# Performance work log

Measured on AMD Instinct MI355X. Metric: run time of the kernel, lower is better.

Reference implementation:

```python
import jax, jax.numpy as jnp
import numpy as np

B, D, E, K = 32768, 512, 64, 4
NCTX = 16
H = (NCTX // 2 - 1) * 768  # 5376: per-expert context block, (n_ctx/2 - 1) rows of ctx_dim=768
NOISE_EPS = 1e-2
LOSS_COEF = 1e-2


def setup_inputs() -> dict:
    key = jax.random.key(0)
    ks = jax.random.split(key, 5)
    x = jax.random.normal(ks[0], (B, D), jnp.float32)
    w_gate = jax.random.normal(ks[1], (D, E), jnp.float32) * 0.02
    w_noise = jax.random.normal(ks[2], (D, E), jnp.float32) * 0.02
    noise = jax.random.normal(ks[3], (B, E), jnp.float32)
    ctx_c = jax.random.normal(ks[4], (E, H), jnp.float32) * 0.02
    return {"x": x, "w_gate": w_gate, "w_noise": w_noise, "noise": noise, "ctx_c": ctx_c}


def _cv_squared(v, eps=1e-10):
    # coefficient-of-variation squared: var / mean^2
    return jnp.var(v) / (jnp.mean(v) ** 2 + eps)


def _normal_cdf(z):
    return 0.5 * (1.0 + jax.lax.erf(z * (1.0 / np.sqrt(2.0))))


def reference(x, w_gate, w_noise, noise, ctx_c):
    # ---- noisy top-k gating (Shazeer sparsely-gated MoE) ----
    clean_logits = x @ w_gate                                    # [B, E]
    noise_stddev = jax.nn.softplus(x @ w_noise) + NOISE_EPS      # [B, E]
    noisy_logits = clean_logits + noise * noise_stddev           # [B, E]

    top_logits, top_idx = jax.lax.top_k(noisy_logits, K + 1)     # [B, K+1]
    top_k_logits = top_logits[:, :K]
    top_k_idx = top_idx[:, :K]
    top_k_gates = jax.nn.softmax(top_k_logits, axis=-1)          # [B, K]

    rows = jnp.arange(B)[:, None]
    gates = jnp.zeros((B, E), x.dtype).at[rows, top_k_idx].set(top_k_gates)  # sparse -> dense scatter

    # ---- load-balancing aux loss ----
    importance = gates.sum(axis=0)                               # [E]
    thr_in = top_logits[:, K][:, None]                           # (K+1)-th largest noisy logit
    thr_out = top_logits[:, K - 1][:, None]                      # K-th largest noisy logit
    is_in = noisy_logits > thr_in
    prob_in = _normal_cdf((clean_logits - thr_in) / noise_stddev)
    prob_out = _normal_cdf((clean_logits - thr_out) / noise_stddev)
    load = jnp.where(is_in, prob_in, prob_out).sum(axis=0)       # [E]
    aux_loss = (_cv_squared(importance) + _cv_squared(load)) * LOSS_COEF

    # ---- weighted combine of per-expert context vectors (as in LPromptLearner) ----
    out = jnp.einsum('be,eh->bh', gates, ctx_c)                  # [B, H]
    return out, aux_loss
```

## Files before the change

kernel.cpp:

```cpp
#include <hip/hip_runtime.h>
#include <math.h>

#define B_ 32768
#define D_ 512
#define E_ 64
#define H_ 5376
#define H4_ (H_ / 4)
#define HC_ 128
#define NCH_ (H_ / HC_)

typedef float f32x4 __attribute__((ext_vector_type(4)));
typedef _Float16 f16x8 __attribute__((ext_vector_type(8)));
typedef unsigned int u32x4 __attribute__((ext_vector_type(4)));

__device__ __forceinline__ unsigned short f16bits(_Float16 h) {
    union { _Float16 h; unsigned short u; } c; c.h = h; return c.u;
}

__global__ __launch_bounds__(256) void prep_kernel(
    const float* __restrict__ wgate, const float* __restrict__ wnoise,
    _Float16* __restrict__ wt0, _Float16* __restrict__ wt1)
{
    int e = blockIdx.x;
    int n  = e >> 4, le = e & 15;
    const float* src = (e < E_) ? (wgate + e) : (wnoise + (e - E_));
    for (int k = threadIdx.x; k < D_; k += 256) {
        float v = src[(size_t)k * E_] * 1024.0f;
        _Float16 h0 = (_Float16)v;
        _Float16 h1 = (_Float16)(v - (float)h0);
        int ks = k >> 5, g = (k & 31) >> 3, j = k & 7;
        size_t idx = ((size_t)(ks * 8 + n) * 64 + g * 16 + le) * 8 + j;
        wt0[idx] = h0;
        wt1[idx] = h1;
    }
}

#define TOP5_STEP(TV, TI)                                              \
    {                                                                  \
        double bm = v0; int bj = 0;                                    \
        if (v1 > bm) { bm = v1; bj = 1; }                              \
        if (v2 > bm) { bm = v2; bj = 2; }                              \
        if (v3 > bm) { bm = v3; bj = 3; }                              \
        int be = bj * 16 + le;                                         \
        _Pragma("unroll")                                              \
        for (int off = 1; off < 16; off <<= 1) {                       \
            double om = __shfl_xor(bm, off, 64);                       \
            int    oe = __shfl_xor(be, off, 64);                       \
            if (om > bm || (om == bm && oe < be)) { bm = om; be = oe; }\
        }                                                              \
        TV = bm; TI = be;                                              \
        bool wn = ((be & 15) == le); int sl = be >> 4;                 \
        v0 = (wn && sl == 0) ? -1.0e300 : v0;                          \
        v1 = (wn && sl == 1) ? -1.0e300 : v1;                          \
        v2 = (wn && sl == 2) ? -1.0e300 : v2;                          \
        v3 = (wn && sl == 3) ? -1.0e300 : v3;                          \
    }

#define ISSUE_LOADS(Q)                                                         \
    _Pragma("unroll")                                                          \
    for (int i = 0; i < 4; ++i) {                                              \
        int id  = t + 256 * i;                                                 \
        const float* src = x + (size_t)(b0 + (id >> 4)) * D_ + (Q) * 128 +     \
                           (id & 15) * 8;                                      \
        ra[2 * i]     = *(const float4*)src;                                   \
        ra[2 * i + 1] = *(const float4*)(src + 4);                             \
    }

#define CONVERT_WRITE(BUF)                                                     \
    _Pragma("unroll")                                                          \
    for (int i = 0; i < 4; ++i) {                                              \
        int id  = t + 256 * i;                                                 \
        int row = id >> 4;                                                     \
        int c   = id & 15;                                                     \
        float vv[8] = {ra[2*i].x, ra[2*i].y, ra[2*i].z, ra[2*i].w,             \
                       ra[2*i+1].x, ra[2*i+1].y, ra[2*i+1].z, ra[2*i+1].w};    \
        unsigned int hw[4], lw[4];                                             \
        _Pragma("unroll")                                                      \
        for (int p = 0; p < 4; ++p) {                                          \
            float va = vv[2*p] * 16.0f, vb = vv[2*p+1] * 16.0f;                \
            _Float16 a0 = (_Float16)va, b0f = (_Float16)vb;                    \
            _Float16 a1 = (_Float16)((va - (float)a0) * 4096.0f);              \
            _Float16 b1 = (_Float16)((vb - (float)b0f) * 4096.0f);             \
            hw[p] = (unsigned)f16bits(a0) | ((unsigned)f16bits(b0f) << 16);    \
            lw[p] = (unsigned)f16bits(a1) | ((unsigned)f16bits(b1) << 16);     \
        }                                                                      \
        int addr = (row * 256 + c * 16) ^ ((row & 7) << 4);                    \
        *(u32x4*)((char*)x0s[BUF] + addr) = (u32x4){hw[0], hw[1], hw[2], hw[3]};\
        *(u32x4*)((char*)x1s[BUF] + addr) = (u32x4){lw[0], lw[1], lw[2], lw[3]};\
    }

__global__ __launch_bounds__(256) void gate_kernel(
    const float* __restrict__ x,
    const _Float16* __restrict__ wt0,
    const _Float16* __restrict__ wt1,
    const float* __restrict__ noise,
    unsigned int* __restrict__ o_idx,
    float4* __restrict__ o_g,
    float* __restrict__ g_imp,
    float* __restrict__ g_load)
{
    __shared__ __align__(16) _Float16 x0s[2][64 * 128];
    __shared__ __align__(16) _Float16 x1s[2][64 * 128];
    __shared__ float s_imp[E_];
    __shared__ float s_load[E_];

    const int t  = threadIdx.x;
    const int w  = t >> 6;
    const int l  = t & 63;
    const int le = l & 15;
    const int g  = l >> 4;
    const int b0 = blockIdx.x * 64;
    const int arow = w * 16 + le;

    if (t < E_) { s_imp[t] = 0.0f; s_load[t] = 0.0f; }

    f32x4 accAC[8], accB[8];
#pragma unroll
    for (int n = 0; n < 8; ++n) {
        accAC[n] = (f32x4){0.f, 0.f, 0.f, 0.f};
        accB[n]  = (f32x4){0.f, 0.f, 0.f, 0.f};
    }

    float4 ra[8];
    ISSUE_LOADS(0)
    CONVERT_WRITE(0)

#pragma unroll
    for (int q = 0; q < 4; ++q) {
        if (q < 3) ISSUE_LOADS(q + 1)
        __syncthreads();
#pragma unroll
        for (int s = 0; s < 4; ++s) {
            int aoff = (arow * 256 + s * 64 + g * 16) ^ ((arow & 7) << 4);
            f16x8 a0 = *(const f16x8*)((const char*)x0s[q & 1] + aoff);
            f16x8 a1 = *(const f16x8*)((const char*)x1s[q & 1] + aoff);
            int ks = q * 4 + s;
#pragma unroll
            for (int n = 0; n < 8; ++n) {
                size_t boff = ((size_t)(ks * 8 + n) * 64 + l) * 8;
                f16x8 b0 = *(const f16x8*)(wt0 + boff);
                f16x8 b1 = *(const f16x8*)(wt1 + boff);
                accAC[n] = __builtin_amdgcn_mfma_f32_16x16x32_f16(a0, b0, accAC[n], 0, 0, 0);
                accAC[n] = __builtin_amdgcn_mfma_f32_16x16x32_f16(a0, b1, accAC[n], 0, 0, 0);
                accB[n]  = __builtin_amdgcn_mfma_f32_16x16x32_f16(a1, b0, accB[n],  0, 0, 0);
            }
        }
        if (q < 3) CONVERT_WRITE((q + 1) & 1)
    }

    const double UNSCALE = 1.0 / 16384.0;
    const double RESC    = 1.0 / 4096.0;
    float loadacc[4] = {0.f, 0.f, 0.f, 0.f};
#pragma unroll
    for (int r = 0; r < 4; ++r) {
        int li = w * 16 + g * 4 + r;
        int b  = b0 + li;
        double cl[4], ny[4];
        float  sdf[4];
#pragma unroll
        for (int n = 0; n < 4; ++n) {
            cl[n] = ((double)accAC[n][r] + (double)accB[n][r] * RESC) * UNSCALE;
            float z = (float)(((double)accAC[n+4][r] + (double)accB[n+4][r] * RESC) * UNSCALE);
            float sp = (z > 20.0f) ? z : log1pf(expf(z));
            sdf[n] = sp + 0.01f;
            float nz = noise[(size_t)b * E_ + le + 16 * n];
            ny[n] = cl[n] + (double)(nz * sdf[n]);
        }
        double v0 = ny[0], v1 = ny[1], v2 = ny[2], v3 = ny[3];
        double tv0, tv1, tv2, tv3, tv4;
        int    ti0, ti1, ti2, ti3, ti4;
        TOP5_STEP(tv0, ti0)
        TOP5_STEP(tv1, ti1)
        TOP5_STEP(tv2, ti2)
        TOP5_STEP(tv3, ti3)
        TOP5_STEP(tv4, ti4)
        float e1 = expf((float)(tv1 - tv0)),
              e2 = expf((float)(tv2 - tv0)),
              e3 = expf((float)(tv3 - tv0));
        float inv = 1.0f / (1.0f + e1 + e2 + e3);
        float g0 = inv, g1 = e1 * inv, g2 = e2 * inv, g3 = e3 * inv;
        if (le == 0) {
            o_idx[b] = (unsigned)ti0 | ((unsigned)ti1 << 8) |
                       ((unsigned)ti2 << 16) | ((unsigned)ti3 << 24);
            float4 gv; gv.x = g0; gv.y = g1; gv.z = g2; gv.w = g3;
            o_g[b] = gv;
            atomicAdd(&s_imp[ti0], g0);
            atomicAdd(&s_imp[ti1], g1);
            atomicAdd(&s_imp[ti2], g2);
            atomicAdd(&s_imp[ti3], g3);
        }
        double thr_out = tv3;
        double thr_in  = tv4;
#pragma unroll
        for (int n = 0; n < 4; ++n) {
            double thr = (ny[n] > thr_in) ? thr_in : thr_out;
            float  zz  = (float)(cl[n] - thr) / sdf[n];
            loadacc[n] += 0.5f * (1.0f + erff(zz * 0.70710678118654752f));
        }
    }
#pragma unroll
    for (int n = 0; n < 4; ++n) atomicAdd(&s_load[16 * n + le], loadacc[n]);
    __syncthreads();
    if (t < E_) {
        atomicAdd(&g_imp[t],  s_imp[t]);
        atomicAdd(&g_load[t], s_load[t]);
    }
}

__global__ __launch_bounds__(256) void dispatch_kernel(
    const float* __restrict__ ctx,
    const unsigned int* __restrict__ o_idx,
    const float4* __restrict__ o_g,
    float* __restrict__ out)
{
    __shared__ f32x4 cs[E_ * (HC_ / 4)];

    const int t  = threadIdx.x;
    const int h0 = blockIdx.x * HC_;
    const int tb = blockIdx.y * 64;

#pragma unroll
    for (int i = 0; i < 8; ++i) {
        int idx = t + 256 * i;
        int e = idx >> 5, c = idx & 31;
        cs[idx] = *(const f32x4*)&ctx[(size_t)e * H_ + h0 + c * 4];
    }
    __syncthreads();

    const int tok = t >> 5;
    const int c   = t & 31;
#pragma unroll
    for (int s = 0; s < 8; ++s) {
        int b = tb + s * 8 + tok;
        unsigned pk = o_idx[b];
        float4 g = o_g[b];
        f32x4 r = g.x * cs[((pk      ) & 255u) * 32 + c]
                + g.y * cs[((pk >>  8) & 255u) * 32 + c]
                + g.z * cs[((pk >> 16) & 255u) * 32 + c]
                + g.w * cs[( pk >> 24         ) * 32 + c];
        __builtin_nontemporal_store(r, (f32x4*)&out[(size_t)b * H_ + h0 + c * 4]);
    }
}

__global__ void loss_kernel(const float* __restrict__ g_imp,
                            const float* __restrict__ g_load,
                            float* __restrict__ out)
{
    int e = threadIdx.x;
    double vi = (double)g_imp[e];
    double vl = (double)g_load[e];
    double si = vi, sl = vl;
#pragma unroll
    for (int off = 1; off < 64; off <<= 1) {
        si += __shfl_xor(si, off, 64);
        sl += __shfl_xor(sl, off, 64);
    }
    double mi = si / 64.0, ml = sl / 64.0;
    double di = vi - mi, dl = vl - ml;
    double qi = di * di, ql = dl * dl;
#pragma unroll
    for (int off = 1; off < 64; off <<= 1) {
        qi += __shfl_xor(qi, off, 64);
        ql += __shfl_xor(ql, off, 64);
    }
    double vari = qi / 64.0, varl = ql / 64.0;
    double cv2i = vari / (mi * mi + 1e-10);
    double cv2l = varl / (ml * ml + 1e-10);
    if (e == 0) out[(size_t)B_ * H_] = (float)((cv2i + cv2l) * 0.01);
}

extern "C" void kernel_launch(void* const* d_in, const int* in_sizes, int n_in,
                              void* d_out, int out_size, void* d_ws, size_t ws_size,
                              hipStream_t stream)
{
    const float* x      = (const float*)d_in[0];
    const float* wgate  = (const float*)d_in[1];
    const float* wnoise = (const float*)d_in[2];
    const float* noise  = (const float*)d_in[3];
    const float* ctx    = (const float*)d_in[4];
    float* out    = (float*)d_out;
    float* g_imp  = (float*)d_ws;
    float* g_load = g_imp + E_;
    _Float16* wt0 = (_Float16*)(g_load + E_);
    _Float16* wt1 = wt0 + 128 * D_;
    unsigned int* o_idx = (unsigned int*)(wt1 + 128 * D_);
    float4* o_g = (float4*)(o_idx + B_);

    (void)hipMemsetAsync(d_ws, 0, 2 * E_ * sizeof(float), stream);
    prep_kernel<<<128, 256, 0, stream>>>(wgate, wnoise, wt0, wt1);
    gate_kernel<<<B_ / 64, 256, 0, stream>>>(x, wt0, wt1, noise,
                                             o_idx, o_g, g_imp, g_load);
    dispatch_kernel<<<dim3(NCH_, B_ / 64), 256, 0, stream>>>(ctx, o_idx, o_g, out);
    loss_kernel<<<1, 64, 0, stream>>>(g_imp, g_load, out);
}
```

Baseline: 197.9 us.

## Fuse gating and expert-context combine into one kernel with per-wave tiles

Merges the dispatch kernel into the gating kernel. Each block now writes the combined context rows for its own 64 tokens straight from the top-k indices and gates, which are held in shared memory, so the o_idx/o_g round trip through global memory and one launch go away. The x staging is restructured so each wave loads and converts its own 16 rows, which lets the block-wide barriers in the k-loop be dropped. The output write now runs in only 512 blocks with one wave per token row, reading ctx from global/L2 instead of an LDS tile. That may lower write-bandwidth parallelism relative to the separate wide-grid dispatch.

```diff
diff --git a/kernel.cpp b/kernel.cpp
--- a/kernel.cpp
+++ b/kernel.cpp
@@ -6,8 +6,6 @@
 #define E_ 64
 #define H_ 5376
 #define H4_ (H_ / 4)
-#define HC_ 128
-#define NCH_ (H_ / HC_)
 
 typedef float f32x4 __attribute__((ext_vector_type(4)));
 typedef _Float16 f16x8 __attribute__((ext_vector_type(8)));
@@ -59,9 +57,9 @@
 #define ISSUE_LOADS(Q)                                                         \
     _Pragma("unroll")                                                          \
     for (int i = 0; i < 4; ++i) {                                              \
-        int id  = t + 256 * i;                                                 \
-        const float* src = x + (size_t)(b0 + (id >> 4)) * D_ + (Q) * 128 +     \
-                           (id & 15) * 8;                                      \
+        int id  = l + 64 * i;                                                  \
+        const float* src = x + (size_t)(b0 + w * 16 + (id >> 4)) * D_ +        \
+                           (Q) * 128 + (id & 15) * 8;                          \
         ra[2 * i]     = *(const float4*)src;                                   \
         ra[2 * i + 1] = *(const float4*)(src + 4);                             \
     }
@@ -69,8 +67,8 @@
 #define CONVERT_WRITE(BUF)                                                     \
     _Pragma("unroll")                                                          \
     for (int i = 0; i < 4; ++i) {                                              \
-        int id  = t + 256 * i;                                                 \
-        int row = id >> 4;                                                     \
+        int id  = l + 64 * i;                                                  \
+        int row = id >> 4;                                    \
         int c   = id & 15;                                                     \
         float vv[8] = {ra[2*i].x, ra[2*i].y, ra[2*i].z, ra[2*i].w,             \
                        ra[2*i+1].x, ra[2*i+1].y, ra[2*i+1].z, ra[2*i+1].w};    \
@@ -85,24 +83,28 @@
             lw[p] = (unsigned)f16bits(a1) | ((unsigned)f16bits(b1) << 16);     \
         }                                                                      \
         int addr = (row * 256 + c * 16) ^ ((row & 7) << 4);                    \
-        *(u32x4*)((char*)x0s[BUF] + addr) = (u32x4){hw[0], hw[1], hw[2], hw[3]};\
-        *(u32x4*)((char*)x1s[BUF] + addr) = (u32x4){lw[0], lw[1], lw[2], lw[3]};\
-    }
-
-__global__ __launch_bounds__(256) void gate_kernel(
+        *(u32x4*)((char*)&x0s[BUF][0] + w * 4096 + addr) =                     \
+            (u32x4){hw[0], hw[1], hw[2], hw[3]};                               \
+        *(u32x4*)((char*)&x1s[BUF][0] + w * 4096 + addr) =                     \
+            (u32x4){lw[0], lw[1], lw[2], lw[3]};                               \
+    }
+
+__global__ __launch_bounds__(256) void gate_out_kernel(
     const float* __restrict__ x,
     const _Float16* __restrict__ wt0,
     const _Float16* __restrict__ wt1,
     const float* __restrict__ noise,
-    unsigned int* __restrict__ o_idx,
-    float4* __restrict__ o_g,
+    const float* __restrict__ ctx,
+    float* __restrict__ out,
     float* __restrict__ g_imp,
     float* __restrict__ g_load)
 {
-    __shared__ __align__(16) _Float16 x0s[2][64 * 128];
-    __shared__ __align__(16) _Float16 x1s[2][64 * 128];
+    __shared__ __align__(16) _Float16 x0s[2][4 * 2048];
+    __shared__ __align__(16) _Float16 x1s[2][4 * 2048];
     __shared__ float s_imp[E_];
     __shared__ float s_load[E_];
+    __shared__ int   s_idx[64][4];
+    __shared__ float s_g[64][4];
 
     const int t  = threadIdx.x;
     const int w  = t >> 6;
@@ -110,9 +112,9 @@
     const int le = l & 15;
     const int g  = l >> 4;
     const int b0 = blockIdx.x * 64;
-    const int arow = w * 16 + le;
 
     if (t < E_) { s_imp[t] = 0.0f; s_load[t] = 0.0f; }
+    __syncthreads();
 
     f32x4 accAC[8], accB[8];
 #pragma unroll
@@ -128,12 +130,11 @@
 #pragma unroll
     for (int q = 0; q < 4; ++q) {
         if (q < 3) ISSUE_LOADS(q + 1)
-        __syncthreads();
 #pragma unroll
         for (int s = 0; s < 4; ++s) {
-            int aoff = (arow * 256 + s * 64 + g * 16) ^ ((arow & 7) << 4);
-            f16x8 a0 = *(const f16x8*)((const char*)x0s[q & 1] + aoff);
-            f16x8 a1 = *(const f16x8*)((const char*)x1s[q & 1] + aoff);
+            int aoff = (le * 256 + s * 64 + g * 16) ^ ((le & 7) << 4);
+            f16x8 a0 = *(const f16x8*)((const char*)&x0s[q & 1][0] + w * 4096 + aoff);
+            f16x8 a1 = *(const f16x8*)((const char*)&x1s[q & 1][0] + w * 4096 + aoff);
             int ks = q * 4 + s;
 #pragma unroll
             for (int n = 0; n < 8; ++n) {
@@ -180,10 +181,9 @@
         float inv = 1.0f / (1.0f + e1 + e2 + e3);
         float g0 = inv, g1 = e1 * inv, g2 = e2 * inv, g3 = e3 * inv;
         if (le == 0) {
-            o_idx[b] = (unsigned)ti0 | ((unsigned)ti1 << 8) |
-                       ((unsigned)ti2 << 16) | ((unsigned)ti3 << 24);
-            float4 gv; gv.x = g0; gv.y = g1; gv.z = g2; gv.w = g3;
-            o_g[b] = gv;
+            s_idx[li][0] = ti0; s_idx[li][1] = ti1;
+            s_idx[li][2] = ti2; s_idx[li][3] = ti3;
+            s_g[li][0] = g0; s_g[li][1] = g1; s_g[li][2] = g2; s_g[li][3] = g3;
             atomicAdd(&s_imp[ti0], g0);
             atomicAdd(&s_imp[ti1], g1);
             atomicAdd(&s_imp[ti2], g2);
@@ -200,45 +200,28 @@
     }
 #pragma unroll
     for (int n = 0; n < 4; ++n) atomicAdd(&s_load[16 * n + le], loadacc[n]);
+
+#pragma unroll 1
+    for (int li16 = 0; li16 < 16; ++li16) {
+        int li = w * 16 + li16;
+        int b  = b0 + li;
+        int   i0 = s_idx[li][0], i1 = s_idx[li][1], i2 = s_idx[li][2], i3 = s_idx[li][3];
+        float gg0 = s_g[li][0], gg1 = s_g[li][1], gg2 = s_g[li][2], gg3 = s_g[li][3];
+        const f32x4* c0 = (const f32x4*)&ctx[(size_t)i0 * H_];
+        const f32x4* c1 = (const f32x4*)&ctx[(size_t)i1 * H_];
+        const f32x4* c2 = (const f32x4*)&ctx[(size_t)i2 * H_];
+        const f32x4* c3 = (const f32x4*)&ctx[(size_t)i3 * H_];
+        f32x4* ob = (f32x4*)&out[(size_t)b * H_];
+        for (int f = l; f < H4_; f += 64) {
+            f32x4 r = gg0 * c0[f] + gg1 * c1[f] + gg2 * c2[f] + gg3 * c3[f];
+            __builtin_nontemporal_store(r, &ob[f]);
+        }
+    }
+
     __syncthreads();
     if (t < E_) {
         atomicAdd(&g_imp[t],  s_imp[t]);
         atomicAdd(&g_load[t], s_load[t]);
-    }
-}
-
-__global__ __launch_bounds__(256) void dispatch_kernel(
-    const float* __restrict__ ctx,
-    const unsigned int* __restrict__ o_idx,
-    const float4* __restrict__ o_g,
-    float* __restrict__ out)
-{
-    __shared__ f32x4 cs[E_ * (HC_ / 4)];
-
-    const int t  = threadIdx.x;
-    const int h0 = blockIdx.x * HC_;
-    const int tb = blockIdx.y * 64;
-
-#pragma unroll
-    for (int i = 0; i < 8; ++i) {
-        int idx = t + 256 * i;
-        int e = idx >> 5, c = idx & 31;
-        cs[idx] = *(const f32x4*)&ctx[(size_t)e * H_ + h0 + c * 4];
-    }
-    __syncthreads();
-
-    const int tok = t >> 5;
-    const int c   = t & 31;
-#pragma unroll
-    for (int s = 0; s < 8; ++s) {
-        int b = tb + s * 8 + tok;
-        unsigned pk = o_idx[b];
-        float4 g = o_g[b];
-        f32x4 r = g.x * cs[((pk      ) & 255u) * 32 + c]
-                + g.y * cs[((pk >>  8) & 255u) * 32 + c]
-                + g.z * cs[((pk >> 16) & 255u) * 32 + c]
-                + g.w * cs[( pk >> 24         ) * 32 + c];
-        __builtin_nontemporal_store(r, (f32x4*)&out[(size_t)b * H_ + h0 + c * 4]);
     }
 }
 
@@ -283,13 +266,10 @@
     float* g_load = g_imp + E_;
     _Float16* wt0 = (_Float16*)(g_load + E_);
     _Float16* wt1 = wt0 + 128 * D_;
-    unsigned int* o_idx = (unsigned int*)(wt1 + 128 * D_);
-    float4* o_g = (float4*)(o_idx + B_);
 
     (void)hipMemsetAsync(d_ws, 0, 2 * E_ * sizeof(float), stream);
     prep_kernel<<<128, 256, 0, stream>>>(wgate, wnoise, wt0, wt1);
-    gate_kernel<<<B_ / 64, 256, 0, stream>>>(x, wt0, wt1, noise,
-                                             o_idx, o_g, g_imp, g_load);
-    dispatch_kernel<<<dim3(NCH_, B_ / 64), 256, 0, stream>>>(ctx, o_idx, o_g, out);
+    gate_out_kernel<<<B_ / 64, 256, 0, stream>>>(x, wt0, wt1, noise, ctx,
+                                                 out, g_imp, g_load);
     loss_kernel<<<1, 64, 0, stream>>>(g_imp, g_load, out);
 }
```

New measurement: 213.4 us. 1.08x slower.
